# Performance work log

Measured on AMD Instinct MI355X. Metric: run time of the kernel, lower is better.

Reference implementation:

```python
import jax, jax.numpy as jnp
import numpy as np

B, T, D = 8, 1024, 1024
H, G = 16, 4            # num_heads, query_groups
HD = D // H             # head_dim = 64
REP = H // G            # heads_per_group
EPS = 1e-10
NEG = -1e9


def setup_inputs() -> dict:
    key = jax.random.key(0)
    k1, k2, k3 = jax.random.split(key, 3)
    x = jax.random.normal(k1, (B, T, D), dtype=jnp.float32)
    w_qkv = jax.random.normal(k2, (D, H * HD + 2 * G * HD), dtype=jnp.float32) * (D ** -0.5)
    w_o = jax.random.normal(k3, (D, D), dtype=jnp.float32) * (D ** -0.5)
    padding_mask = jnp.ones((B, T), dtype=bool)
    return {"x": x, "w_qkv": w_qkv, "w_o": w_o, "padding_mask": padding_mask}


def _l2_norm(t):
    # qk_norm_type=2: L2 normalize over head_dim
    return t / (jnp.sqrt(jnp.sum(t * t, axis=-1, keepdims=True)) + EPS)


def reference(x, w_qkv, w_o, padding_mask):
    # fused QKV projection: [B,T,D] @ [D, H*HD + 2*G*HD]
    qkv = x @ w_qkv
    q, k, v = jnp.split(qkv, [H * HD, H * HD + G * HD], axis=-1)
    q = q.reshape(B, T, H, HD)
    k = k.reshape(B, T, G, HD)
    v = v.reshape(B, T, G, HD)
    # QK normalization (L2 over head_dim)
    q = _l2_norm(q)
    k = _l2_norm(k)
    # GQA: expand KV heads (repeat_interleave along head dim)
    k = jnp.repeat(k, REP, axis=2)  # [B,T,H,HD]
    v = jnp.repeat(v, REP, axis=2)
    # to [B,H,T,HD]
    q = q.transpose(0, 2, 1, 3)
    k = k.transpose(0, 2, 1, 3)
    v = v.transpose(0, 2, 1, 3)
    # causal + padding mask, True = attend
    causal = jnp.tril(jnp.ones((T, T), dtype=bool))  # [T_q, T_k]
    valid = padding_mask[:, None, :, None] & padding_mask[:, None, None, :] & causal[None, None]
    scale = HD ** -0.5  # SDPA default scale
    scores = jnp.einsum('bhqd,bhkd->bhqk', q, k) * scale
    scores = jnp.where(valid, scores, NEG)
    attn = jax.nn.softmax(scores, axis=-1)
    out = jnp.einsum('bhqk,bhkd->bhqd', attn, v)  # [B,H,T,HD]
    out = out.transpose(0, 2, 1, 3).reshape(B, T, D)
    return out @ w_o
```

## Files before the change

kernel.cpp:

```cpp
#include <hip/hip_runtime.h>
#include <hip/hip_bf16.h>

typedef __attribute__((ext_vector_type(8))) short short8;
typedef __attribute__((ext_vector_type(4))) short short4v;
typedef __attribute__((ext_vector_type(4))) float f32x4;

#define B_ 8
#define T_ 1024
#define D_ 1024
#define H_ 16
#define G_ 4
#define HD_ 64
#define QKVW 1536
#define KSTEPS 32

#define GLOAD16(gp, lp) __builtin_amdgcn_global_load_lds( \
    (const __attribute__((address_space(1))) void*)(gp),  \
    (__attribute__((address_space(3))) void*)(lp), 16, 0, 0)

__device__ __forceinline__ float exp2_fast(float x) {
    return __builtin_amdgcn_exp2f(x);
}

__device__ __forceinline__ short8 pack_bf16x8(float4 a, float4 b) {
    union { short8 s; __hip_bfloat16 h[8]; } u;
    u.h[0] = __float2bfloat16(a.x); u.h[1] = __float2bfloat16(a.y);
    u.h[2] = __float2bfloat16(a.z); u.h[3] = __float2bfloat16(a.w);
    u.h[4] = __float2bfloat16(b.x); u.h[5] = __float2bfloat16(b.y);
    u.h[6] = __float2bfloat16(b.z); u.h[7] = __float2bfloat16(b.w);
    return u.s;
}

__global__ __launch_bounds__(256) void cvt_transpose(
    const float* __restrict__ in, __hip_bfloat16* __restrict__ outT, int K, int N)
{
    __shared__ float tile[32][33];
    const int k0 = blockIdx.y * 32, n0 = blockIdx.x * 32;
    const int r = threadIdx.x >> 5, c = threadIdx.x & 31;
    #pragma unroll
    for (int i = 0; i < 4; ++i)
        tile[r + i * 8][c] = in[(size_t)(k0 + r + i * 8) * N + n0 + c];
    __syncthreads();
    #pragma unroll
    for (int i = 0; i < 4; ++i)
        outT[(size_t)(n0 + r + i * 8) * K + k0 + c] = __float2bfloat16(tile[c][r + i * 8]);
}

__global__ __launch_bounds__(256) void gemm_qkv(
    const float* __restrict__ Af,
    const __hip_bfloat16* __restrict__ Bt,
    __hip_bfloat16* __restrict__ qkv,
    __hip_bfloat16* __restrict__ vt)
{
    const int M = B_ * T_, K = D_;
    __shared__ __hip_bfloat16 As[3][128 * 32];
    __shared__ __hip_bfloat16 Bs[3][128 * 32];

    const int tid  = threadIdx.x;
    const int lane = tid & 63;
    const int wr   = (tid >> 6) >> 1;
    const int wc   = (tid >> 6) & 1;

    const int rpx = (M >> 7) >> 3;
    const int xcd = blockIdx.x & 7;
    const int lin = blockIdx.x >> 3;
    const int by  = xcd * rpx + (lin % rpx);
    const int bx  = lin / rpx;
    const int m0 = by * 128;
    const int n0 = bx * 128;

    f32x4 acc[4][4] = {};

    const int sr0 = tid >> 2;
    const int sr1 = 64 + sr0;
    const int slot  = (tid & 3) ^ ((tid >> 3) & 3);
    const int sc_ln = (tid & 3) * 8;
    const int sc_sw = slot * 8;
    const int ws0 = sr0 * 64 + slot * 16;
    const int ws1 = sr1 * 64 + slot * 16;

    const float* Ar0f = Af + (size_t)(m0 + sr0) * K + sc_ln;
    const float* Ar1f = Af + (size_t)(m0 + sr1) * K + sc_ln;
    const __hip_bfloat16* Br0 = Bt + (size_t)(n0 + sr0) * K + sc_sw;
    const __hip_bfloat16* Br1 = Bt + (size_t)(n0 + sr1) * K + sc_sw;

    const int fr = lane & 15;
    const int kb = (lane >> 4) * 16;
    const int swzg = ((fr >> 1) & 3) << 4;

    float4 ra[2][4];

    auto stageB = [&](int t) {
        GLOAD16(Br0 + t * 32, (char*)&Bs[t % 3][0] + tid * 16);
        GLOAD16(Br1 + t * 32, (char*)&Bs[t % 3][0] + 4096 + tid * 16);
    };
    auto loadA = [&](int t) {
        ra[t & 1][0] = *(const float4*)(Ar0f + t * 32);
        ra[t & 1][1] = *(const float4*)(Ar0f + t * 32 + 4);
        ra[t & 1][2] = *(const float4*)(Ar1f + t * 32);
        ra[t & 1][3] = *(const float4*)(Ar1f + t * 32 + 4);
    };
    auto writeA = [&](int t) {
        *(short8*)((char*)&As[t % 3][0] + ws0) = pack_bf16x8(ra[t & 1][0], ra[t & 1][1]);
        *(short8*)((char*)&As[t % 3][0] + ws1) = pack_bf16x8(ra[t & 1][2], ra[t & 1][3]);
    };

    stageB(0); loadA(0);
    stageB(1); loadA(1);
    writeA(0);
    asm volatile("s_waitcnt lgkmcnt(0)" ::: "memory");
    asm volatile("s_waitcnt vmcnt(6)" ::: "memory");
    __builtin_amdgcn_s_barrier();
    __builtin_amdgcn_sched_barrier(0);

    #pragma unroll
    for (int t = 0; t < KSTEPS; ++t) {
        if (t + 2 < KSTEPS) { stageB(t + 2); loadA(t + 2); }

        short8 a[4], b[4];
        #pragma unroll
        for (int m = 0; m < 4; ++m)
            a[m] = *(const short8*)((char*)&As[t % 3][0] +
                    (wr * 64 + m * 16 + fr) * 64 + (kb ^ swzg));
        #pragma unroll
        for (int n = 0; n < 4; ++n)
            b[n] = *(const short8*)((char*)&Bs[t % 3][0] +
                    (wc * 64 + n * 16 + fr) * 64 + (kb ^ swzg));
        #pragma unroll
        for (int m = 0; m < 4; ++m)
            #pragma unroll
            for (int n = 0; n < 4; ++n)
                acc[m][n] = __builtin_amdgcn_mfma_f32_16x16x32_bf16(a[m], b[n], acc[m][n], 0, 0, 0);

        if (t + 1 < KSTEPS) {
            writeA(t + 1);
            asm volatile("s_waitcnt lgkmcnt(0)" ::: "memory");
            if (t + 2 < KSTEPS)
                asm volatile("s_waitcnt vmcnt(6)" ::: "memory");
            else
                asm volatile("s_waitcnt vmcnt(0)" ::: "memory");
            __builtin_amdgcn_s_barrier();
            __builtin_amdgcn_sched_barrier(0);
        }
    }

    const int rowb  = m0 + wr * 64 + (lane >> 4) * 4;
    const int colb0 = n0 + wc * 64;

    if (n0 < 1280) {
        const float extra = (n0 < 1024) ? 0.18033688f : 1.0f;
        #pragma unroll
        for (int m = 0; m < 4; ++m)
            #pragma unroll
            for (int r = 0; r < 4; ++r) {
                float ss = 0.f;
                #pragma unroll
                for (int n = 0; n < 4; ++n) { float v = acc[m][n][r]; ss += v * v; }
                ss += __shfl_xor(ss, 1, 64);
                ss += __shfl_xor(ss, 2, 64);
                ss += __shfl_xor(ss, 4, 64);
                ss += __shfl_xor(ss, 8, 64);
                float sc = extra / (sqrtf(ss) + 1e-10f);
                const size_t rbase = (size_t)(rowb + m * 16 + r) * QKVW + colb0 + fr;
                #pragma unroll
                for (int n = 0; n < 4; ++n)
                    qkv[rbase + n * 16] = __float2bfloat16(acc[m][n][r] * sc);
            }
    } else {
        #pragma unroll
        for (int m = 0; m < 4; ++m) {
            const int row = rowb + m * 16;
            const int bb  = row >> 10;
            const int t0  = row & 1023;
            #pragma unroll
            for (int n = 0; n < 4; ++n) {
                const int cv = colb0 + fr + n * 16 - 1280;
                const int gg = cv >> 6, d = cv & 63;
                union { short4v s; __hip_bfloat16 h[4]; } u;
                u.h[0] = __float2bfloat16(acc[m][n][0]);
                u.h[1] = __float2bfloat16(acc[m][n][1]);
                u.h[2] = __float2bfloat16(acc[m][n][2]);
                u.h[3] = __float2bfloat16(acc[m][n][3]);
                *reinterpret_cast<short4v*>(
                    vt + ((size_t)((bb * G_ + gg) * HD_ + d)) * T_ + t0) = u.s;
            }
        }
    }
}

__global__ __launch_bounds__(256) void gemm_tn_f32(
    const __hip_bfloat16* __restrict__ A,
    const __hip_bfloat16* __restrict__ Bt,
    float* __restrict__ C, int M, int N, int K)
{
    __shared__ __hip_bfloat16 As[3][128 * 32];
    __shared__ __hip_bfloat16 Bs[3][128 * 32];

    const int tid  = threadIdx.x;
    const int lane = tid & 63;
    const int wr   = (tid >> 6) >> 1;
    const int wc   = (tid >> 6) & 1;

    const int rpx = (M >> 7) >> 3;
    const int xcd = blockIdx.x & 7;
    const int lin = blockIdx.x >> 3;
    const int by  = xcd * rpx + (lin % rpx);
    const int bx  = lin / rpx;
    const int m0 = by * 128;
    const int n0 = bx * 128;

    f32x4 acc[4][4] = {};

    const int sr0 = tid >> 2;
    const int sr1 = 64 + sr0;
    const int slot  = (tid & 3) ^ ((tid >> 3) & 3);
    const int sc_sw = slot * 8;

    const __hip_bfloat16* Ar0 = A  + (size_t)(m0 + sr0) * K + sc_sw;
    const __hip_bfloat16* Ar1 = A  + (size_t)(m0 + sr1) * K + sc_sw;
    const __hip_bfloat16* Br0 = Bt + (size_t)(n0 + sr0) * K + sc_sw;
    const __hip_bfloat16* Br1 = Bt + (size_t)(n0 + sr1) * K + sc_sw;

    const int fr = lane & 15;
    const int kb = (lane >> 4) * 16;
    const int swzg = ((fr >> 1) & 3) << 4;

    auto stage = [&](int t) {
        GLOAD16(Ar0 + t * 32, (char*)&As[t % 3][0] + tid * 16);
        GLOAD16(Ar1 + t * 32, (char*)&As[t % 3][0] + 4096 + tid * 16);
        GLOAD16(Br0 + t * 32, (char*)&Bs[t % 3][0] + tid * 16);
        GLOAD16(Br1 + t * 32, (char*)&Bs[t % 3][0] + 4096 + tid * 16);
    };

    stage(0);
    stage(1);
    asm volatile("s_waitcnt vmcnt(4)" ::: "memory");
    __builtin_amdgcn_s_barrier();
    __builtin_amdgcn_sched_barrier(0);

    #pragma unroll
    for (int t = 0; t < KSTEPS; ++t) {
        if (t + 2 < KSTEPS) stage(t + 2);

        short8 a[4], b[4];
        #pragma unroll
        for (int m = 0; m < 4; ++m)
            a[m] = *(const short8*)((char*)&As[t % 3][0] +
                    (wr * 64 + m * 16 + fr) * 64 + (kb ^ swzg));
        #pragma unroll
        for (int n = 0; n < 4; ++n)
            b[n] = *(const short8*)((char*)&Bs[t % 3][0] +
                    (wc * 64 + n * 16 + fr) * 64 + (kb ^ swzg));
        #pragma unroll
        for (int m = 0; m < 4; ++m)
            #pragma unroll
            for (int n = 0; n < 4; ++n)
                acc[m][n] = __builtin_amdgcn_mfma_f32_16x16x32_bf16(a[m], b[n], acc[m][n], 0, 0, 0);

        if (t + 1 < KSTEPS) {
            if (t + 2 < KSTEPS)
                asm volatile("s_waitcnt vmcnt(4)" ::: "memory");
            else
                asm volatile("s_waitcnt vmcnt(0)" ::: "memory");
            __builtin_amdgcn_s_barrier();
            __builtin_amdgcn_sched_barrier(0);
        }
    }

    const int rowb = m0 + wr * 64 + (lane >> 4) * 4;
    const int colb = n0 + wc * 64 + fr;
    #pragma unroll
    for (int m = 0; m < 4; ++m)
        #pragma unroll
        for (int n = 0; n < 4; ++n)
            #pragma unroll
            for (int r = 0; r < 4; ++r)
                C[(size_t)(rowb + m * 16 + r) * N + colb + n * 16] = acc[m][n][r];
}

__global__ __launch_bounds__(256) void attn_fwd(
    const __hip_bfloat16* __restrict__ qkv,
    const __hip_bfloat16* __restrict__ vt,
    __hip_bfloat16* __restrict__ out)
{
    const int pair = blockIdx.x;
    const int h  = blockIdx.y;
    const int b  = blockIdx.z;
    const int g  = h >> 2;

    const int tid  = threadIdx.x;
    const int lane = tid & 63;
    const int wid  = tid >> 6;

    __shared__ __hip_bfloat16 Ks[2 * 4096];
    __shared__ __hip_bfloat16 Vs[2 * 4096];
    __shared__ __hip_bfloat16 Ps[4 * 2048];

    const int fr  = lane & 15;
    const int kf  = (lane >> 4) * 8;
    const int kb  = kf * 2;
    const int swz = (fr & 7) << 4;

    const int srow = tid >> 3;
    const int scol = ((tid & 7) * 8) ^ ((srow & 7) << 3);

    const size_t kgbase = (size_t)(b * T_) * QKVW + H_ * HD_ + g * HD_ + scol;
    const size_t vgbase = (size_t)((b * G_ + g) * HD_) * T_ + scol;

    char* PsB = (char*)Ps + wid * 4096;

    auto stage = [&](int kt, int sl) {
        GLOAD16(qkv + kgbase + (size_t)(kt * 64 + srow) * QKVW,
                (char*)Ks + sl * 8192 + tid * 16);
        GLOAD16(qkv + kgbase + (size_t)(kt * 64 + 32 + srow) * QKVW,
                (char*)Ks + sl * 8192 + 4096 + tid * 16);
        GLOAD16(vt + vgbase + (size_t)srow * T_ + kt * 64,
                (char*)Vs + sl * 8192 + tid * 16);
        GLOAD16(vt + vgbase + (size_t)(32 + srow) * T_ + kt * 64,
                (char*)Vs + sl * 8192 + 4096 + tid * 16);
    };

    for (int half = 0; half < 2; ++half) {
        const int qt  = half ? (7 - pair) : pair;
        const int q0  = qt * 128;
        const int nkt = 2 * qt + 2;

        short8 qf[2][2];
        #pragma unroll
        for (int m = 0; m < 2; ++m) {
            const size_t qbase =
                ((size_t)(b * T_ + q0 + wid * 32 + m * 16 + fr)) * QKVW + h * HD_;
            qf[m][0] = *(const short8*)(qkv + qbase + kf);
            qf[m][1] = *(const short8*)(qkv + qbase + 32 + kf);
        }
        const int rb0 = q0 + wid * 32 + (lane >> 4) * 4;

        float lsum[2][4] = {};
        f32x4 o[2][4] = {};

        for (int kt = 0; kt < nkt; kt += 2) {
            stage(kt, 0);
            stage(kt + 1, 1);
            __syncthreads();

            #pragma unroll
            for (int sl = 0; sl < 2; ++sl) {
                const int  ck  = kt + sl;
                const bool msk = (ck >= nkt - 2);
                char* KsB = (char*)Ks + sl * 8192;
                char* VsB = (char*)Vs + sl * 8192;

                short8 bk0[4], bk1[4];
                #pragma unroll
                for (int nf = 0; nf < 4; ++nf) {
                    const int row = fr + 16 * nf;
                    bk0[nf] = *(const short8*)(KsB + row * 128 + (kb ^ swz));
                    bk1[nf] = *(const short8*)(KsB + row * 128 + ((64 + kb) ^ swz));
                }

                #pragma unroll
                for (int m = 0; m < 2; ++m) {
                    f32x4 s[4] = {};
                    __builtin_amdgcn_s_setprio(1);
                    #pragma unroll
                    for (int nf = 0; nf < 4; ++nf) {
                        s[nf] = __builtin_amdgcn_mfma_f32_16x16x32_bf16(qf[m][0], bk0[nf], s[nf], 0, 0, 0);
                        s[nf] = __builtin_amdgcn_mfma_f32_16x16x32_bf16(qf[m][1], bk1[nf], s[nf], 0, 0, 0);
                    }
                    __builtin_amdgcn_s_setprio(0);

                    if (msk) {
                        #pragma unroll
                        for (int nf = 0; nf < 4; ++nf) {
                            int col = ck * 64 + fr + 16 * nf;
                            #pragma unroll
                            for (int r = 0; r < 4; ++r) {
                                float p = (col <= rb0 + m * 16 + r) ? exp2_fast(s[nf][r]) : 0.f;
                                lsum[m][r] += p;
                                int q = m * 16 + (lane >> 4) * 4 + r;
                                *(__hip_bfloat16*)(PsB + q * 128 +
                                    ((2 * (fr + 16 * nf)) ^ ((q & 7) << 4))) = __float2bfloat16(p);
                            }
                        }
                    } else {
                        #pragma unroll
                        for (int nf = 0; nf < 4; ++nf)
                            #pragma unroll
                            for (int r = 0; r < 4; ++r) {
                                float p = exp2_fast(s[nf][r]);
                                lsum[m][r] += p;
                                int q = m * 16 + (lane >> 4) * 4 + r;
                                *(__hip_bfloat16*)(PsB + q * 128 +
                                    ((2 * (fr + 16 * nf)) ^ ((q & 7) << 4))) = __float2bfloat16(p);
                            }
                    }
                }

                short8 bv0[4], bv1[4];
                #pragma unroll
                for (int nf = 0; nf < 4; ++nf) {
                    const int row = fr + 16 * nf;
                    bv0[nf] = *(const short8*)(VsB + row * 128 + (kb ^ swz));
                    bv1[nf] = *(const short8*)(VsB + row * 128 + ((64 + kb) ^ swz));
                }
                __builtin_amdgcn_s_setprio(1);
                #pragma unroll
                for (int m = 0; m < 2; ++m) {
                    short8 pa0 = *(const short8*)(PsB + (m * 16 + fr) * 128 + (kb ^ swz));
                    short8 pa1 = *(const short8*)(PsB + (m * 16 + fr) * 128 + ((64 + kb) ^ swz));
                    #pragma unroll
                    for (int nf = 0; nf < 4; ++nf) {
                        o[m][nf] = __builtin_amdgcn_mfma_f32_16x16x32_bf16(pa0, bv0[nf], o[m][nf], 0, 0, 0);
                        o[m][nf] = __builtin_amdgcn_mfma_f32_16x16x32_bf16(pa1, bv1[nf], o[m][nf], 0, 0, 0);
                    }
                }
                __builtin_amdgcn_s_setprio(0);
            }
            __syncthreads();
        }

        #pragma unroll
        for (int m = 0; m < 2; ++m) {
            float linv[4];
            #pragma unroll
            for (int r = 0; r < 4; ++r) {
                float v = lsum[m][r];
                v += __shfl_xor(v, 1, 64);
                v += __shfl_xor(v, 2, 64);
                v += __shfl_xor(v, 4, 64);
                v += __shfl_xor(v, 8, 64);
                linv[r] = 1.0f / v;
            }
            #pragma unroll
            for (int nf = 0; nf < 4; ++nf) {
                int col = fr + 16 * nf;
                #pragma unroll
                for (int r = 0; r < 4; ++r) {
                    float v = o[m][nf][r] * linv[r];
                    out[((size_t)(b * T_ + rb0 + m * 16 + r)) * (H_ * HD_) + h * HD_ + col] =
                        __float2bfloat16(v);
                }
            }
        }
    }
}

extern "C" void kernel_launch(void* const* d_in, const int* in_sizes, int n_in,
                              void* d_out, int out_size, void* d_ws, size_t ws_size,
                              hipStream_t stream) {
    const float* x_f     = (const float*)d_in[0];
    const float* w_qkv_f = (const float*)d_in[1];
    const float* w_o_f   = (const float*)d_in[2];
    float* out = (float*)d_out;

    const int NX  = B_ * T_ * D_;
    const int NWQ = D_ * QKVW;
    const int NWO = D_ * D_;

    __hip_bfloat16* attn_out = (__hip_bfloat16*)d_ws;
    __hip_bfloat16* wqkvT = attn_out + NX;
    __hip_bfloat16* woT   = wqkvT + NWQ;
    __hip_bfloat16* qkv   = woT + NWO;
    __hip_bfloat16* vt    = qkv + (size_t)(B_ * T_) * QKVW;

    dim3 blk(256);

    cvt_transpose<<<dim3(QKVW / 32, D_ / 32), blk, 0, stream>>>(w_qkv_f, wqkvT, D_, QKVW);
    cvt_transpose<<<dim3(D_ / 32, D_ / 32), blk, 0, stream>>>(w_o_f, woT, D_, D_);

    gemm_qkv<<<dim3((QKVW / 128) * ((B_ * T_) / 128)), blk, 0, stream>>>(
        x_f, wqkvT, qkv, vt);

    attn_fwd<<<dim3(4, H_, B_), blk, 0, stream>>>(qkv, vt, attn_out);

    gemm_tn_f32<<<dim3((D_ / 128) * ((B_ * T_) / 128)), blk, 0, stream>>>(
        attn_out, woT, out, B_ * T_, D_, D_);
}
```

Baseline: 116.5 us.

## Use 4-stage LDS ring with two k-steps per barrier in GEMMs; merge weight transposes

```diff
diff --git a/kernel.cpp b/kernel.cpp
--- a/kernel.cpp
+++ b/kernel.cpp
@@ -31,11 +31,19 @@
     return u.s;
 }
 
-__global__ __launch_bounds__(256) void cvt_transpose(
-    const float* __restrict__ in, __hip_bfloat16* __restrict__ outT, int K, int N)
+__global__ __launch_bounds__(256) void cvt_transpose2(
+    const float* __restrict__ w_qkv, const float* __restrict__ w_o,
+    __hip_bfloat16* __restrict__ wqkvT, __hip_bfloat16* __restrict__ woT)
 {
+    const int z = blockIdx.z;
+    const int N = z ? D_ : QKVW;
+    const int n0 = blockIdx.x * 32;
+    if (n0 >= N) return;
+    const float* in = z ? w_o : w_qkv;
+    __hip_bfloat16* outT = z ? woT : wqkvT;
+
     __shared__ float tile[32][33];
-    const int k0 = blockIdx.y * 32, n0 = blockIdx.x * 32;
+    const int k0 = blockIdx.y * 32;
     const int r = threadIdx.x >> 5, c = threadIdx.x & 31;
     #pragma unroll
     for (int i = 0; i < 4; ++i)
@@ -43,7 +51,7 @@
     __syncthreads();
     #pragma unroll
     for (int i = 0; i < 4; ++i)
-        outT[(size_t)(n0 + r + i * 8) * K + k0 + c] = __float2bfloat16(tile[c][r + i * 8]);
+        outT[(size_t)(n0 + r + i * 8) * D_ + k0 + c] = __float2bfloat16(tile[c][r + i * 8]);
 }
 
 __global__ __launch_bounds__(256) void gemm_qkv(
@@ -53,8 +61,8 @@
     __hip_bfloat16* __restrict__ vt)
 {
     const int M = B_ * T_, K = D_;
-    __shared__ __hip_bfloat16 As[3][128 * 32];
-    __shared__ __hip_bfloat16 Bs[3][128 * 32];
+    __shared__ __hip_bfloat16 As[4][128 * 32];
+    __shared__ __hip_bfloat16 Bs[4][128 * 32];
 
     const int tid  = threadIdx.x;
     const int lane = tid & 63;
@@ -91,8 +99,8 @@
     float4 ra[2][4];
 
     auto stageB = [&](int t) {
-        GLOAD16(Br0 + t * 32, (char*)&Bs[t % 3][0] + tid * 16);
-        GLOAD16(Br1 + t * 32, (char*)&Bs[t % 3][0] + 4096 + tid * 16);
+        GLOAD16(Br0 + t * 32, (char*)&Bs[t & 3][0] + tid * 16);
+        GLOAD16(Br1 + t * 32, (char*)&Bs[t & 3][0] + 4096 + tid * 16);
     };
     auto loadA = [&](int t) {
         ra[t & 1][0] = *(const float4*)(Ar0f + t * 32);
@@ -101,47 +109,40 @@
         ra[t & 1][3] = *(const float4*)(Ar1f + t * 32 + 4);
     };
     auto writeA = [&](int t) {
-        *(short8*)((char*)&As[t % 3][0] + ws0) = pack_bf16x8(ra[t & 1][0], ra[t & 1][1]);
-        *(short8*)((char*)&As[t % 3][0] + ws1) = pack_bf16x8(ra[t & 1][2], ra[t & 1][3]);
-    };
-
-    stageB(0); loadA(0);
-    stageB(1); loadA(1);
-    writeA(0);
-    asm volatile("s_waitcnt lgkmcnt(0)" ::: "memory");
-    asm volatile("s_waitcnt vmcnt(6)" ::: "memory");
-    __builtin_amdgcn_s_barrier();
-    __builtin_amdgcn_sched_barrier(0);
-
-    #pragma unroll
-    for (int t = 0; t < KSTEPS; ++t) {
-        if (t + 2 < KSTEPS) { stageB(t + 2); loadA(t + 2); }
-
+        *(short8*)((char*)&As[t & 3][0] + ws0) = pack_bf16x8(ra[t & 1][0], ra[t & 1][1]);
+        *(short8*)((char*)&As[t & 3][0] + ws1) = pack_bf16x8(ra[t & 1][2], ra[t & 1][3]);
+    };
+    auto computeStep = [&](int t) {
         short8 a[4], b[4];
         #pragma unroll
         for (int m = 0; m < 4; ++m)
-            a[m] = *(const short8*)((char*)&As[t % 3][0] +
+            a[m] = *(const short8*)((char*)&As[t & 3][0] +
                     (wr * 64 + m * 16 + fr) * 64 + (kb ^ swzg));
         #pragma unroll
         for (int n = 0; n < 4; ++n)
-            b[n] = *(const short8*)((char*)&Bs[t % 3][0] +
+            b[n] = *(const short8*)((char*)&Bs[t & 3][0] +
                     (wc * 64 + n * 16 + fr) * 64 + (kb ^ swzg));
         #pragma unroll
         for (int m = 0; m < 4; ++m)
             #pragma unroll
             for (int n = 0; n < 4; ++n)
                 acc[m][n] = __builtin_amdgcn_mfma_f32_16x16x32_bf16(a[m], b[n], acc[m][n], 0, 0, 0);
-
-        if (t + 1 < KSTEPS) {
-            writeA(t + 1);
-            asm volatile("s_waitcnt lgkmcnt(0)" ::: "memory");
-            if (t + 2 < KSTEPS)
-                asm volatile("s_waitcnt vmcnt(6)" ::: "memory");
-            else
-                asm volatile("s_waitcnt vmcnt(0)" ::: "memory");
-            __builtin_amdgcn_s_barrier();
-            __builtin_amdgcn_sched_barrier(0);
-        }
+    };
+
+    stageB(0); stageB(1);
+    loadA(0);  writeA(0);
+    loadA(1);  writeA(1);
+    __syncthreads();
+
+    #pragma unroll
+    for (int t = 0; t < KSTEPS; t += 2) {
+        const bool more = (t + 2 < KSTEPS);
+        if (more) { stageB(t + 2); stageB(t + 3); loadA(t + 2); }
+        computeStep(t);
+        if (more) { writeA(t + 2); loadA(t + 3); }
+        computeStep(t + 1);
+        if (more) writeA(t + 3);
+        __syncthreads();
     }
 
     const int rowb  = m0 + wr * 64 + (lane >> 4) * 4;
@@ -193,8 +194,8 @@
     const __hip_bfloat16* __restrict__ Bt,
     float* __restrict__ C, int M, int N, int K)
 {
-    __shared__ __hip_bfloat16 As[3][128 * 32];
-    __shared__ __hip_bfloat16 Bs[3][128 * 32];
+    __shared__ __hip_bfloat16 As[4][128 * 32];
+    __shared__ __hip_bfloat16 Bs[4][128 * 32];
 
     const int tid  = threadIdx.x;
     const int lane = tid & 63;
@@ -226,45 +227,37 @@
     const int swzg = ((fr >> 1) & 3) << 4;
 
     auto stage = [&](int t) {
-        GLOAD16(Ar0 + t * 32, (char*)&As[t % 3][0] + tid * 16);
-        GLOAD16(Ar1 + t * 32, (char*)&As[t % 3][0] + 4096 + tid * 16);
-        GLOAD16(Br0 + t * 32, (char*)&Bs[t % 3][0] + tid * 16);
-        GLOAD16(Br1 + t * 32, (char*)&Bs[t % 3][0] + 4096 + tid * 16);
-    };
-
-    stage(0);
-    stage(1);
-    asm volatile("s_waitcnt vmcnt(4)" ::: "memory");
-    __builtin_amdgcn_s_barrier();
-    __builtin_amdgcn_sched_barrier(0);
-
-    #pragma unroll
-    for (int t = 0; t < KSTEPS; ++t) {
-        if (t + 2 < KSTEPS) stage(t + 2);
-
+        GLOAD16(Ar0 + t * 32, (char*)&As[t & 3][0] + tid * 16);
+        GLOAD16(Ar1 + t * 32, (char*)&As[t & 3][0] + 4096 + tid * 16);
+        GLOAD16(Br0 + t * 32, (char*)&Bs[t & 3][0] + tid * 16);
+        GLOAD16(Br1 + t * 32, (char*)&Bs[t & 3][0] + 4096 + tid * 16);
+    };
+    auto computeStep = [&](int t) {
         short8 a[4], b[4];
         #pragma unroll
         for (int m = 0; m < 4; ++m)
-            a[m] = *(const short8*)((char*)&As[t % 3][0] +
+            a[m] = *(const short8*)((char*)&As[t & 3][0] +
                     (wr * 64 + m * 16 + fr) * 64 + (kb ^ swzg));
         #pragma unroll
         for (int n = 0; n < 4; ++n)
-            b[n] = *(const short8*)((char*)&Bs[t % 3][0] +
+            b[n] = *(const short8*)((char*)&Bs[t & 3][0] +
                     (wc * 64 + n * 16 + fr) * 64 + (kb ^ swzg));
         #pragma unroll
         for (int m = 0; m < 4; ++m)
             #pragma unroll
             for (int n = 0; n < 4; ++n)
                 acc[m][n] = __builtin_amdgcn_mfma_f32_16x16x32_bf16(a[m], b[n], acc[m][n], 0, 0, 0);
-
-        if (t + 1 < KSTEPS) {
-            if (t + 2 < KSTEPS)
-                asm volatile("s_waitcnt vmcnt(4)" ::: "memory");
-            else
-                asm volatile("s_waitcnt vmcnt(0)" ::: "memory");
-            __builtin_amdgcn_s_barrier();
-            __builtin_amdgcn_sched_barrier(0);
-        }
+    };
+
+    stage(0); stage(1);
+    __syncthreads();
+
+    #pragma unroll
+    for (int t = 0; t < KSTEPS; t += 2) {
+        if (t + 2 < KSTEPS) { stage(t + 2); stage(t + 3); }
+        computeStep(t);
+        computeStep(t + 1);
+        __syncthreads();
     }
 
     const int rowb = m0 + wr * 64 + (lane >> 4) * 4;
@@ -465,8 +458,8 @@
 
     dim3 blk(256);
 
-    cvt_transpose<<<dim3(QKVW / 32, D_ / 32), blk, 0, stream>>>(w_qkv_f, wqkvT, D_, QKVW);
-    cvt_transpose<<<dim3(D_ / 32, D_ / 32), blk, 0, stream>>>(w_o_f, woT, D_, D_);
+    cvt_transpose2<<<dim3(QKVW / 32, D_ / 32, 2), blk, 0, stream>>>(
+        w_qkv_f, w_o_f, wqkvT, woT);
 
     gemm_qkv<<<dim3((QKVW / 128) * ((B_ * T_) / 128)), blk, 0, stream>>>(
         x_f, wqkvT, qkv, vt);
```

Measured after the change: 134.3 us. 15.3% more time.
